# Kernel tuning notes

Hardware: AMD Instinct MI355X
Metric: run time of the kernel (lower is better)

The kernel has to match this reference:

```python
import jax, jax.numpy as jnp
import numpy as np

N = 50000      # nodes
E = 800000     # edges (avg degree 16)
G = 128        # g_dim (input feature dim)
H1 = 128       # h1_dim (RGCN output dim)
H2 = 32        # h2_dim (per-head channels)
HEADS = 4
R = 6          # num_relations
OUT = H2 * HEADS  # 128, BatchNorm width
BN_EPS = 1e-5


def setup_inputs() -> dict:
    key = jax.random.key(0)
    k = jax.random.split(key, 16)
    s = 0.05
    return {
        "node_features": jax.random.normal(k[0], (N, G), jnp.float32),
        "node_type": jax.random.randint(k[1], (N,), 0, 3),
        "edge_index": jax.random.randint(k[2], (2, E), 0, N),
        "edge_type": jax.random.randint(k[3], (E,), 0, R),
        # RGCNConv params (root_weight=True, bias=True, aggr='mean')
        "W_rel": jax.random.normal(k[4], (R, G, H1), jnp.float32) * s,
        "W_root": jax.random.normal(k[5], (G, H1), jnp.float32) * s,
        "b_rgcn": jnp.zeros((H1,), jnp.float32),
        # TransformerConv params (concat=True, root_weight=True via lin_skip)
        "Wq": jax.random.normal(k[6], (H1, OUT), jnp.float32) * s,
        "bq": jnp.zeros((OUT,), jnp.float32),
        "Wk": jax.random.normal(k[7], (H1, OUT), jnp.float32) * s,
        "bk": jnp.zeros((OUT,), jnp.float32),
        "Wv": jax.random.normal(k[8], (H1, OUT), jnp.float32) * s,
        "bv": jnp.zeros((OUT,), jnp.float32),
        "Wskip": jax.random.normal(k[9], (H1, OUT), jnp.float32) * s,
        "bskip": jnp.zeros((OUT,), jnp.float32),
        # BatchNorm1d affine params
        "bn_gamma": jnp.ones((OUT,), jnp.float32),
        "bn_beta": jnp.zeros((OUT,), jnp.float32),
    }


def _gnn_forward(node_features, edge_index, edge_type,
                 W_rel, W_root, b_rgcn,
                 Wq, bq, Wk, bk, Wv, bv, Wskip, bskip,
                 bn_gamma, bn_beta):
    src, dst = edge_index[0], edge_index[1]  # message flows src (j) -> dst (i)

    # ---- RGCNConv with mean aggregation per relation ----
    # Transform all nodes under every relation: [R, N, H1]
    xt = jnp.einsum('nd,rdo->rno', node_features, W_rel)
    msg = xt[edge_type, src]                          # [E, H1]
    seg = edge_type * N + dst                         # composite (relation, dst) segment id
    agg = jax.ops.segment_sum(msg, seg, num_segments=R * N).reshape(R, N, H1)
    cnt = jax.ops.segment_sum(jnp.ones((E,), msg.dtype), seg,
                              num_segments=R * N).reshape(R, N)
    x = node_features @ W_root + b_rgcn + (agg / jnp.maximum(cnt, 1.0)[:, :, None]).sum(0)

    # ---- TransformerConv (heads=HEADS, concat=True) ----
    q = (x @ Wq + bq).reshape(N, HEADS, H2)
    kk = (x @ Wk + bk).reshape(N, HEADS, H2)
    v = (x @ Wv + bv).reshape(N, HEADS, H2)

    score = (q[dst] * kk[src]).sum(-1) / np.sqrt(H2)  # [E, HEADS]
    m = jax.ops.segment_max(score, dst, num_segments=N)   # -inf for isolated nodes
    m = jnp.where(jnp.isfinite(m), m, 0.0)
    ex = jnp.exp(score - m[dst])
    den = jax.ops.segment_sum(ex, dst, num_segments=N)
    alpha = ex / (den[dst] + 1e-16)                   # [E, HEADS]

    out = jax.ops.segment_sum(alpha[:, :, None] * v[src], dst,
                              num_segments=N).reshape(N, OUT)
    out = out + x @ Wskip + bskip                     # skip / root connection

    # ---- BatchNorm1d (training-mode batch stats) + LeakyReLU(0.01) ----
    mu = out.mean(0)
    var = out.var(0)  # biased, as torch uses for normalization
    y = (out - mu) * jax.lax.rsqrt(var + BN_EPS) * bn_gamma + bn_beta
    return jax.nn.leaky_relu(y, negative_slope=0.01)


def reference(node_features, node_type, edge_index, edge_type,
              W_rel, W_root, b_rgcn,
              Wq, bq, Wk, bk, Wv, bv, Wskip, bskip,
              bn_gamma, bn_beta):
    # node_type is accepted but unused, matching the original forward.
    return _gnn_forward(node_features, edge_index, edge_type,
                        W_rel, W_root, b_rgcn,
                        Wq, bq, Wk, bk, Wv, bv, Wskip, bskip,
                        bn_gamma, bn_beta)
```

## Files before the change

### kernel.cpp

```cpp
#include <hip/hip_runtime.h>
#include <hip/hip_fp16.h>
#include <stdint.h>

#define G      128
#define OUTW   128
#define RNUM   6

typedef unsigned short us;
typedef _Float16 f16x8 __attribute__((ext_vector_type(8)));
typedef float    f32x4 __attribute__((ext_vector_type(4)));

__device__ inline float h2f(us u) { __half h; *(us*)&h = u; return __half2float(h); }
__device__ inline us f2h(float f) { __half h = __float2half(f); return *(us*)&h; }

union FragU { f16x8 v; ushort4 u[2]; };

__global__ void count_kernel(const int* __restrict__ ei, const int* __restrict__ et,
                             int* __restrict__ deg, int* __restrict__ cntR,
                             int N, int E) {
    int e = blockIdx.x * blockDim.x + threadIdx.x;
    if (e >= E) return;
    int dst = ei[E + e];
    int r   = et[e];
    atomicAdd(&deg[dst], 1);
    atomicAdd(&cntR[r * N + dst], 1);
}

__global__ __launch_bounds__(256)
void scan_part(const int* __restrict__ deg, int* __restrict__ bsum, int n) {
    __shared__ int s[256];
    int base = blockIdx.x * 1024, t = threadIdx.x;
    int v = 0;
    for (int j = 0; j < 4; ++j) { int idx = base + j * 256 + t; if (idx < n) v += deg[idx]; }
    s[t] = v; __syncthreads();
    for (int off = 128; off; off >>= 1) { if (t < off) s[t] += s[t + off]; __syncthreads(); }
    if (!t) bsum[blockIdx.x] = s[0];
}

__global__ void scan_top(const int* __restrict__ bsum, int* __restrict__ boff,
                         int* __restrict__ rowptr, int nb, int n) {
    int t = threadIdx.x;
    int v = (t < nb) ? bsum[t] : 0;
    for (int off = 1; off < 64; off <<= 1) {
        int y = __shfl_up(v, off);
        if (t >= off) v += y;
    }
    if (t < nb) boff[t + 1] = v;
    if (!t) boff[0] = 0;
    if (t == 63) rowptr[n] = v;
}

__global__ __launch_bounds__(256)
void scan_apply(const int* __restrict__ deg, const int* __restrict__ boff,
                int* __restrict__ rowptr, int* __restrict__ cursor, int n) {
    __shared__ int L[1024];
    __shared__ int SS[256];
    int base = blockIdx.x * 1024, t = threadIdx.x;
    for (int j = 0; j < 4; ++j) { int idx = base + j * 256 + t; L[j * 256 + t] = (idx < n) ? deg[idx] : 0; }
    __syncthreads();
    int s0 = L[t*4] + L[t*4+1] + L[t*4+2] + L[t*4+3];
    SS[t] = s0; __syncthreads();
    for (int off = 1; off < 256; off <<= 1) {
        int y = (t >= off) ? SS[t - off] : 0;
        __syncthreads();
        SS[t] += y;
        __syncthreads();
    }
    int e0 = (t ? SS[t - 1] : 0) + boff[blockIdx.x];
    int4 ov;
    int a;
    a = L[t*4+0]; ov.x = e0; e0 += a;
    a = L[t*4+1]; ov.y = e0; e0 += a;
    a = L[t*4+2]; ov.z = e0; e0 += a;
    a = L[t*4+3]; ov.w = e0; e0 += a;
    int idx0 = base + t * 4;
    if (idx0 + 3 < n) {
        *(int4*)(rowptr + idx0) = ov;
        *(int4*)(cursor + idx0) = ov;
    } else {
        int vals[4] = {ov.x, ov.y, ov.z, ov.w};
        for (int k = 0; k < 4; ++k)
            if (idx0 + k < n) { rowptr[idx0 + k] = vals[k]; cursor[idx0 + k] = vals[k]; }
    }
}

__global__ void scatter_kernel(const int* __restrict__ ei, const int* __restrict__ et,
                               int* __restrict__ cursor, unsigned int* __restrict__ epack,
                               int N, int E) {
    int e = blockIdx.x * blockDim.x + threadIdx.x;
    if (e >= E) return;
    int src = ei[e];
    int dst = ei[E + e];
    int r   = et[e];
    int pos = atomicAdd(&cursor[dst], 1);
    epack[pos] = (unsigned int)src | ((unsigned int)r << 16);
}

__global__ void xhalf_kernel(const float* __restrict__ x, us* __restrict__ xh, int total8) {
    int i = blockIdx.x * blockDim.x + threadIdx.x;
    if (i >= total8) return;
    float4 a = ((const float4*)x)[2*i];
    float4 b = ((const float4*)x)[2*i+1];
    ushort4 u0 = { f2h(a.x), f2h(a.y), f2h(a.z), f2h(a.w) };
    ushort4 u1 = { f2h(b.x), f2h(b.y), f2h(b.z), f2h(b.w) };
    ((ushort4*)xh)[2*i]   = u0;
    ((ushort4*)xh)[2*i+1] = u1;
}

__global__ __launch_bounds__(256)
void wconv_rgcn(const float* __restrict__ Wrel, const float* __restrict__ Wroot,
                ushort4* __restrict__ Btr) {
    int idx = blockIdx.x * 256 + threadIdx.x;
    if (idx >= 224 * 128) return;
    int kq = idx >> 7, n = idx & 127;
    ushort4 o;
    us* op = (us*)&o;
#pragma unroll
    for (int i = 0; i < 4; ++i) {
        int k = 4 * kq + i;
        float v = (k < 768) ? Wrel[(size_t)k * 128 + n] : Wroot[(size_t)(k - 768) * 128 + n];
        op[i] = f2h(v);
    }
    Btr[idx] = o;
}

__global__ __launch_bounds__(256)
void wconv_qkvs(const float* __restrict__ Wq, const float* __restrict__ Wk,
                const float* __restrict__ Wv, const float* __restrict__ Ws,
                ushort4* __restrict__ Btq) {
    int idx = blockIdx.x * 256 + threadIdx.x;
    if (idx >= 32 * 512) return;
    int kq = idx >> 9, n = idx & 511;
    int quad = n >> 7, nl = n & 127;
    const float* W = (quad == 0) ? Wq : (quad == 1) ? Wk : (quad == 2) ? Wv : Ws;
    ushort4 o;
    us* op = (us*)&o;
#pragma unroll
    for (int i = 0; i < 4; ++i) {
        int k = 4 * kq + i;
        op[i] = f2h(W[(size_t)k * 128 + nl]);
    }
    Btq[idx] = o;
}

__global__ __launch_bounds__(256)
void agg_kernel(const us* __restrict__ xh, const int* __restrict__ rowptr,
                const unsigned* __restrict__ epack, const int* __restrict__ cntR,
                us* __restrict__ meanh, int N) {
    const int wv = threadIdx.x >> 6, l = threadIdx.x & 63;
    const int i = blockIdx.x * 4 + wv;
    if (i >= N) return;
    const int e0 = rowptr[i], e1 = rowptr[i + 1];
    float2 a0{0,0}, a1{0,0}, a2{0,0}, a3{0,0}, a4{0,0}, a5{0,0};

#define LOADX(P) (*(const ushort2*)(xh + (size_t)((P) & 0xFFFFu) * G + 2*l))
#define ACC(P, U) { unsigned r_ = (P) >> 16; float vx_ = h2f((U).x), vy_ = h2f((U).y); \
    if      (r_ == 0) { a0.x += vx_; a0.y += vy_; } \
    else if (r_ == 1) { a1.x += vx_; a1.y += vy_; } \
    else if (r_ == 2) { a2.x += vx_; a2.y += vy_; } \
    else if (r_ == 3) { a3.x += vx_; a3.y += vy_; } \
    else if (r_ == 4) { a4.x += vx_; a4.y += vy_; } \
    else              { a5.x += vx_; a5.y += vy_; } }

    for (int base = e0; base < e1; base += 64) {
        const int nc = min(64, e1 - base);
        unsigned pv = 0;
        if (base + l < e1) pv = epack[base + l];
        int j = 0;
        for (; j + 8 <= nc; j += 8) {
            unsigned q0 = (unsigned)__shfl((int)pv, j+0);
            unsigned q1 = (unsigned)__shfl((int)pv, j+1);
            unsigned q2 = (unsigned)__shfl((int)pv, j+2);
            unsigned q3 = (unsigned)__shfl((int)pv, j+3);
            unsigned q4 = (unsigned)__shfl((int)pv, j+4);
            unsigned q5 = (unsigned)__shfl((int)pv, j+5);
            unsigned q6 = (unsigned)__shfl((int)pv, j+6);
            unsigned q7 = (unsigned)__shfl((int)pv, j+7);
            ushort2 u0 = LOADX(q0), u1 = LOADX(q1), u2 = LOADX(q2), u3 = LOADX(q3);
            ushort2 u4 = LOADX(q4), u5 = LOADX(q5), u6 = LOADX(q6), u7 = LOADX(q7);
            ACC(q0,u0); ACC(q1,u1); ACC(q2,u2); ACC(q3,u3);
            ACC(q4,u4); ACC(q5,u5); ACC(q6,u6); ACC(q7,u7);
        }
        for (; j < nc; ++j) {
            unsigned q0 = (unsigned)__shfl((int)pv, j);
            ushort2 u0 = LOADX(q0);
            ACC(q0,u0);
        }
    }
#undef ACC
#undef LOADX

    us* mrow = meanh + (size_t)i * 768 + 2*l;
#define WR(RIDX, A) { \
    float c_ = (float)cntR[(RIDX) * N + i]; \
    float s_ = 1.f / fmaxf(c_, 1.f); \
    ushort2 t_ = { f2h((A).x * s_), f2h((A).y * s_) }; \
    *(ushort2*)(mrow + (RIDX) * G) = t_; }
    WR(0, a0); WR(1, a1); WR(2, a2); WR(3, a3); WR(4, a4); WR(5, a5);
#undef WR
}

__global__ __launch_bounds__(256)
void rgcn_mfma(const us* __restrict__ meanh, const us* __restrict__ xh,
               const ushort4* __restrict__ Btr, const float* __restrict__ brg,
               us* __restrict__ xrh, int N) {
    __shared__ ushort4 Ald[16 * 64];
    const int tid = threadIdx.x;
    const int w = tid >> 6, l = tid & 63;
    const int lh = l >> 4, lm = l & 15;
    const int base = blockIdx.x * 64;
    const int arow = w * 16 + lm;

    f32x4 acc[8];
#pragma unroll
    for (int ct = 0; ct < 8; ++ct) {
        float b = brg[ct * 16 + lm];
        acc[ct] = (f32x4){b, b, b, b};
    }

    const int srow = tid >> 2;
    const int sk0  = (tid & 3) * 16;

    for (int ch = 0; ch < 14; ++ch) {
        int gi = base + srow;
        int4 d0 = {0,0,0,0}, d1 = {0,0,0,0};
        if (gi < N) {
            const us* src = (ch < 12) ? (meanh + (size_t)gi * 768 + ch * 64 + sk0)
                                      : (xh    + (size_t)gi * 128 + (ch - 12) * 64 + sk0);
            d0 = *(const int4*)src;
            d1 = *(const int4*)(src + 8);
        }
        __syncthreads();
        int kqb = sk0 >> 2;
        Ald[(kqb + 0) * 64 + srow] = ((ushort4*)&d0)[0];
        Ald[(kqb + 1) * 64 + srow] = ((ushort4*)&d0)[1];
        Ald[(kqb + 2) * 64 + srow] = ((ushort4*)&d1)[0];
        Ald[(kqb + 3) * 64 + srow] = ((ushort4*)&d1)[1];
        __syncthreads();

#pragma unroll
        for (int s = 0; s < 2; ++s) {
            FragU af;
            int kql = s * 8 + lh;
            af.u[0] = Ald[kql * 64 + arow];
            af.u[1] = Ald[(kql + 4) * 64 + arow];
            int kqg = ch * 16 + s * 8 + lh;
            const ushort4* B0 = Btr + (size_t)kqg * 128;
            const ushort4* B1 = Btr + (size_t)(kqg + 4) * 128;
#pragma unroll
            for (int ct = 0; ct < 8; ++ct) {
                FragU bf;
                bf.u[0] = B0[ct * 16 + lm];
                bf.u[1] = B1[ct * 16 + lm];
                acc[ct] = __builtin_amdgcn_mfma_f32_16x16x32_f16(af.v, bf.v, acc[ct], 0, 0, 0);
            }
        }
    }

#pragma unroll
    for (int ct = 0; ct < 8; ++ct) {
#pragma unroll
        for (int i = 0; i < 4; ++i) {
            int r = base + w * 16 + 4 * lh + i;
            if (r < N) xrh[(size_t)r * 128 + ct * 16 + lm] = f2h(acc[ct][i]);
        }
    }
}

__global__ __launch_bounds__(256)
void qkvs_mfma(const us* __restrict__ xrh, const ushort4* __restrict__ Btq,
               const float* __restrict__ bq, const float* __restrict__ bk,
               const float* __restrict__ bv, const float* __restrict__ bs,
               float* __restrict__ qs, us* __restrict__ kvh, int N) {
    __shared__ ushort4 Ald[32 * 16];
    const int tid = threadIdx.x;
    const int w = tid >> 6, l = tid & 63;
    const int lh = l >> 4, lm = l & 15;
    const int base = blockIdx.x * 16;

    {
        int row = tid >> 4, k0 = (tid & 15) * 8;
        int gi = base + row;
        int4 d0 = {0,0,0,0};
        if (gi < N) d0 = *(const int4*)(xrh + (size_t)gi * 128 + k0);
        int kqb = k0 >> 2;
        Ald[(kqb + 0) * 16 + row] = ((ushort4*)&d0)[0];
        Ald[(kqb + 1) * 16 + row] = ((ushort4*)&d0)[1];
    }
    __syncthreads();

    const float* bias = (w == 0) ? bq : (w == 1) ? bk : (w == 2) ? bv : bs;
    f32x4 acc[8];
#pragma unroll
    for (int ct = 0; ct < 8; ++ct) {
        float b = bias[ct * 16 + lm];
        acc[ct] = (f32x4){b, b, b, b};
    }

#pragma unroll
    for (int s = 0; s < 4; ++s) {
        FragU af;
        int kq = s * 8 + lh;
        af.u[0] = Ald[kq * 16 + lm];
        af.u[1] = Ald[(kq + 4) * 16 + lm];
        const ushort4* B0 = Btq + (size_t)kq * 512 + w * 128;
        const ushort4* B1 = Btq + (size_t)(kq + 4) * 512 + w * 128;
#pragma unroll
        for (int ct = 0; ct < 8; ++ct) {
            FragU bf;
            bf.u[0] = B0[ct * 16 + lm];
            bf.u[1] = B1[ct * 16 + lm];
            acc[ct] = __builtin_amdgcn_mfma_f32_16x16x32_f16(af.v, bf.v, acc[ct], 0, 0, 0);
        }
    }

    if (w == 0 || w == 3) {
        int off = (w == 0) ? 0 : 128;
#pragma unroll
        for (int ct = 0; ct < 8; ++ct)
#pragma unroll
            for (int i = 0; i < 4; ++i) {
                int r = base + 4 * lh + i;
                if (r < N) qs[(size_t)r * 256 + off + ct * 16 + lm] = acc[ct][i];
            }
    } else {
        int off = (w == 1) ? 0 : 2;
#pragma unroll
        for (int ct = 0; ct < 8; ++ct)
#pragma unroll
            for (int i = 0; i < 4; ++i) {
                int r = base + 4 * lh + i;
                int col = ct * 16 + lm;
                if (r < N) kvh[(size_t)r * 256 + (col >> 1) * 4 + (col & 1) + off] = f2h(acc[ct][i]);
            }
    }
}

__global__ __launch_bounds__(256)
void attn_kernel(const float* __restrict__ qs, const us* __restrict__ kvh,
                 const int* __restrict__ rowptr, const unsigned* __restrict__ epack,
                 float* __restrict__ out, int N) {
    const int wv = threadIdx.x >> 6, l = threadIdx.x & 63;
    const int i = blockIdx.x * 4 + wv;
    if (i >= N) return;
    const float QS = 0.17677669529663687f;

    float2 q2 = *(const float2*)(qs + (size_t)i * 256 + 2*l);
    q2.x *= QS; q2.y *= QS;

    float m = -INFINITY, den = 0.f;
    float2 acc = {0.f, 0.f};
    const int e0 = rowptr[i], e1 = rowptr[i + 1];

#define KVLOAD(P) (*(const ushort4*)(kvh + (size_t)((P) & 0xFFFFu) * 256 + 4*l))
#define SCORE(U, S) { \
    float s_ = q2.x * h2f((U).x) + q2.y * h2f((U).y); \
    s_ += __shfl_xor(s_, 1, 16); s_ += __shfl_xor(s_, 2, 16); \
    s_ += __shfl_xor(s_, 4, 16); s_ += __shfl_xor(s_, 8, 16); \
    S = s_; }

    for (int base = e0; base < e1; base += 64) {
        const int nc = min(64, e1 - base);
        unsigned pv = 0;
        if (base + l < e1) pv = epack[base + l];
        int j = 0;
        for (; j + 4 <= nc; j += 4) {
            unsigned p0 = (unsigned)__shfl((int)pv, j+0);
            unsigned p1 = (unsigned)__shfl((int)pv, j+1);
            unsigned p2 = (unsigned)__shfl((int)pv, j+2);
            unsigned p3 = (unsigned)__shfl((int)pv, j+3);
            ushort4 k0 = KVLOAD(p0), k1 = KVLOAD(p1), k2 = KVLOAD(p2), k3 = KVLOAD(p3);
            float s0, s1, s2, s3;
            SCORE(k0, s0); SCORE(k1, s1); SCORE(k2, s2); SCORE(k3, s3);
            float mx = fmaxf(fmaxf(fmaxf(s0, s1), fmaxf(s2, s3)), m);
            float rs = __expf(m - mx);
            float p0e = __expf(s0 - mx), p1e = __expf(s1 - mx);
            float p2e = __expf(s2 - mx), p3e = __expf(s3 - mx);
            den = den * rs + ((p0e + p1e) + (p2e + p3e));
            acc.x = acc.x * rs + p0e*h2f(k0.z) + p1e*h2f(k1.z) + p2e*h2f(k2.z) + p3e*h2f(k3.z);
            acc.y = acc.y * rs + p0e*h2f(k0.w) + p1e*h2f(k1.w) + p2e*h2f(k2.w) + p3e*h2f(k3.w);
            m = mx;
        }
        for (; j < nc; ++j) {
            unsigned p0 = (unsigned)__shfl((int)pv, j);
            ushort4 k0 = KVLOAD(p0);
            float s0; SCORE(k0, s0);
            float mx = fmaxf(m, s0);
            float rs = __expf(m - mx);
            float pe = __expf(s0 - mx);
            den = den * rs + pe;
            acc.x = acc.x * rs + pe * h2f(k0.z);
            acc.y = acc.y * rs + pe * h2f(k0.w);
            m = mx;
        }
    }
#undef SCORE
#undef KVLOAD

    float inv = 1.f / (den + 1e-16f);
    float2 sk = *(const float2*)(qs + (size_t)i * 256 + 128 + 2*l);
    float2 o = { acc.x * inv + sk.x, acc.y * inv + sk.y };
    *(float2*)(out + (size_t)i * OUTW + 2*l) = o;
}

__global__ __launch_bounds__(256)
void bnreduce_kernel(const float* __restrict__ out, float* __restrict__ bnS,
                     float* __restrict__ bnQ, int N) {
    __shared__ float S[256], Q[256];
    const int tid = threadIdx.x;
    const int col = tid & 127, half = tid >> 7;
    float s = 0.f, q = 0.f;
    for (int r = blockIdx.x * 2 + half; r < N; r += gridDim.x * 2) {
        float v = out[(size_t)r * OUTW + col];
        s += v; q += v * v;
    }
    S[tid] = s; Q[tid] = q;
    __syncthreads();
    if (tid < 128) {
        atomicAdd(&bnS[tid], S[tid] + S[tid + 128]);
        atomicAdd(&bnQ[tid], Q[tid] + Q[tid + 128]);
    }
}

__global__ void bnstats_kernel(const float* __restrict__ bnS, const float* __restrict__ bnQ,
                               const float* __restrict__ gamma, const float* __restrict__ beta,
                               float* __restrict__ bnA, float* __restrict__ bnB, int N) {
    int c = threadIdx.x;
    if (c >= 128) return;
    float fN  = (float)N;
    float mu  = bnS[c] / fN;
    float var = bnQ[c] / fN - mu * mu;
    float rv  = rsqrtf(var + 1e-5f);
    float A   = rv * gamma[c];
    bnA[c] = A;
    bnB[c] = beta[c] - mu * A;
}

__global__ void apply_kernel(float* __restrict__ out, const float* __restrict__ bnA,
                             const float* __restrict__ bnB, int total4) {
    int idx4 = blockIdx.x * blockDim.x + threadIdx.x;
    if (idx4 >= total4) return;
    float4 v = ((const float4*)out)[idx4];
    int c0 = (idx4 * 4) & 127;
    float y;
    y = bnA[c0    ] * v.x + bnB[c0    ]; v.x = (y > 0.f) ? y : 0.01f * y;
    y = bnA[c0 + 1] * v.y + bnB[c0 + 1]; v.y = (y > 0.f) ? y : 0.01f * y;
    y = bnA[c0 + 2] * v.z + bnB[c0 + 2]; v.z = (y > 0.f) ? y : 0.01f * y;
    y = bnA[c0 + 3] * v.w + bnB[c0 + 3]; v.w = (y > 0.f) ? y : 0.01f * y;
    ((float4*)out)[idx4] = v;
}

static inline char* alignp(char* p) {
    return (char*)(((uintptr_t)p + 255) & ~(uintptr_t)255);
}

extern "C" void kernel_launch(void* const* d_in, const int* in_sizes, int n_in,
                              void* d_out, int out_size, void* d_ws, size_t ws_size,
                              hipStream_t stream) {
    const float* x     = (const float*)d_in[0];
    const int*   ei    = (const int*)  d_in[2];
    const int*   et    = (const int*)  d_in[3];
    const float* Wrel  = (const float*)d_in[4];
    const float* Wroot = (const float*)d_in[5];
    const float* brg   = (const float*)d_in[6];
    const float* Wq    = (const float*)d_in[7];
    const float* bq    = (const float*)d_in[8];
    const float* Wk    = (const float*)d_in[9];
    const float* bk    = (const float*)d_in[10];
    const float* Wv    = (const float*)d_in[11];
    const float* bv    = (const float*)d_in[12];
    const float* Wsk   = (const float*)d_in[13];
    const float* bsk   = (const float*)d_in[14];
    const float* gamma = (const float*)d_in[15];
    const float* beta  = (const float*)d_in[16];
    float* out = (float*)d_out;

    const int N = in_sizes[0] / G;
    const int E = in_sizes[3];
    const int NB_SCAN = (N + 1023) / 1024;

    char* w = (char*)d_ws;
    int* deg   = (int*)w;            w += (size_t)N * 4;
    int* cntR  = (int*)w;            w += (size_t)RNUM * N * 4;
    float* bnS = (float*)w;          w += 128 * 4;
    float* bnQ = (float*)w;          w += 128 * 4;
    float* bnA = (float*)w;          w += 128 * 4;
    float* bnB = (float*)w;          w += 128 * 4;
    size_t zero_bytes = (size_t)(w - (char*)d_ws);
    w = alignp(w);
    int* bsum  = (int*)w;            w += 64 * 4;
    int* boff  = (int*)w;            w += 65 * 4;
    w = alignp(w);
    int* rowptr = (int*)w;           w += (size_t)(N + 1) * 4;
    w = alignp(w);
    int* cursor = (int*)w;           w += (size_t)N * 4;
    w = alignp(w);
    unsigned* epack = (unsigned*)w;  w += (size_t)E * 4;
    w = alignp(w);
    us* xh     = (us*)w;             w += (size_t)N * G * 2;
    w = alignp(w);
    us* xrh    = (us*)w;             w += (size_t)N * OUTW * 2;
    w = alignp(w);
    ushort4* Btr = (ushort4*)w;      w += (size_t)224 * 128 * 8;
    w = alignp(w);
    ushort4* Btq = (ushort4*)w;      w += (size_t)32 * 512 * 8;
    w = alignp(w);
    us*    meanh = (us*)w;
    float* qs    = (float*)w;
    us*    kvh   = (us*)(w + (size_t)N * 256 * 4);

    hipMemsetAsync(d_ws, 0, zero_bytes, stream);

    int eb = (E + 255) / 256;
    count_kernel<<<eb, 256, 0, stream>>>(ei, et, deg, cntR, N, E);

    scan_part<<<NB_SCAN, 256, 0, stream>>>(deg, bsum, N);
    scan_top<<<1, 64, 0, stream>>>(bsum, boff, rowptr, NB_SCAN, N);
    scan_apply<<<NB_SCAN, 256, 0, stream>>>(deg, boff, rowptr, cursor, N);

    scatter_kernel<<<eb, 256, 0, stream>>>(ei, et, cursor, epack, N, E);

    int total8 = N * G / 8;
    xhalf_kernel<<<(total8 + 255) / 256, 256, 0, stream>>>(x, xh, total8);

    wconv_rgcn<<<112, 256, 0, stream>>>(Wrel, Wroot, Btr);
    wconv_qkvs<<<64, 256, 0, stream>>>(Wq, Wk, Wv, Wsk, Btq);

    agg_kernel<<<(N + 3) / 4, 256, 0, stream>>>(xh, rowptr, epack, cntR, meanh, N);

    rgcn_mfma<<<(N + 63) / 64, 256, 0, stream>>>(meanh, xh, Btr, brg, xrh, N);

    qkvs_mfma<<<(N + 15) / 16, 256, 0, stream>>>(xrh, Btq, bq, bk, bv, bsk, qs, kvh, N);

    attn_kernel<<<(N + 3) / 4, 256, 0, stream>>>(qs, kvh, rowptr, epack, out, N);

    bnreduce_kernel<<<200, 256, 0, stream>>>(out, bnS, bnQ, N);
    bnstats_kernel<<<1, 128, 0, stream>>>(bnS, bnQ, gamma, beta, bnA, bnB, N);

    int total4 = N * OUTW / 4;
    apply_kernel<<<(total4 + 255) / 256, 256, 0, stream>>>(out, bnA, bnB, total4);
}
```

Measured before the change: 509.8 us.

## Sort edges by (dst, relation) and fuse RGCN aggregation into MFMA kernel

Edges are now bucketed into CSR segments keyed by (dst, relation), which replaces the per-edge relation branch and the separate per-relation count array. The mean aggregation is moved into the RGCN MFMA kernel, so each block gathers neighbour features straight into LDS tiles per relation chunk. This removes the intermediate meanh buffer of 768 halves per node and one kernel launch. In exchange the CSR is six times larger, the scan grows to a 512-thread top level, and each wave walks edges serially with scalar readfirstlane loads, which lowers gather parallelism inside the MFMA kernel.

```diff
diff --git a/kernel.cpp b/kernel.cpp
--- a/kernel.cpp
+++ b/kernel.cpp
@@ -16,47 +16,51 @@
 union FragU { f16x8 v; ushort4 u[2]; };
 
 __global__ void count_kernel(const int* __restrict__ ei, const int* __restrict__ et,
-                             int* __restrict__ deg, int* __restrict__ cntR,
-                             int N, int E) {
+                             int* __restrict__ segcnt, int N, int E) {
     int e = blockIdx.x * blockDim.x + threadIdx.x;
     if (e >= E) return;
     int dst = ei[E + e];
     int r   = et[e];
-    atomicAdd(&deg[dst], 1);
-    atomicAdd(&cntR[r * N + dst], 1);
-}
-
-__global__ __launch_bounds__(256)
-void scan_part(const int* __restrict__ deg, int* __restrict__ bsum, int n) {
+    atomicAdd(&segcnt[dst * RNUM + r], 1);
+}
+
+__global__ __launch_bounds__(256)
+void scan_part(const int* __restrict__ cnt, int* __restrict__ bsum, int n) {
     __shared__ int s[256];
     int base = blockIdx.x * 1024, t = threadIdx.x;
     int v = 0;
-    for (int j = 0; j < 4; ++j) { int idx = base + j * 256 + t; if (idx < n) v += deg[idx]; }
+    for (int j = 0; j < 4; ++j) { int idx = base + j * 256 + t; if (idx < n) v += cnt[idx]; }
     s[t] = v; __syncthreads();
     for (int off = 128; off; off >>= 1) { if (t < off) s[t] += s[t + off]; __syncthreads(); }
     if (!t) bsum[blockIdx.x] = s[0];
 }
 
-__global__ void scan_top(const int* __restrict__ bsum, int* __restrict__ boff,
-                         int* __restrict__ rowptr, int nb, int n) {
+__global__ __launch_bounds__(512)
+void scan_top(const int* __restrict__ bsum, int* __restrict__ boff,
+              int* __restrict__ segptr, int nb, int n) {
+    __shared__ int s[512];
     int t = threadIdx.x;
     int v = (t < nb) ? bsum[t] : 0;
-    for (int off = 1; off < 64; off <<= 1) {
-        int y = __shfl_up(v, off);
-        if (t >= off) v += y;
-    }
-    if (t < nb) boff[t + 1] = v;
+    s[t] = v;
+    __syncthreads();
+    for (int off = 1; off < 512; off <<= 1) {
+        int y = (t >= off) ? s[t - off] : 0;
+        __syncthreads();
+        s[t] += y;
+        __syncthreads();
+    }
+    if (t < nb) boff[t + 1] = s[t];
     if (!t) boff[0] = 0;
-    if (t == 63) rowptr[n] = v;
-}
-
-__global__ __launch_bounds__(256)
-void scan_apply(const int* __restrict__ deg, const int* __restrict__ boff,
-                int* __restrict__ rowptr, int* __restrict__ cursor, int n) {
+    if (t == nb - 1) segptr[n] = s[t];
+}
+
+__global__ __launch_bounds__(256)
+void scan_apply(const int* __restrict__ cnt, const int* __restrict__ boff,
+                int* __restrict__ segptr, int* __restrict__ cursor, int n) {
     __shared__ int L[1024];
     __shared__ int SS[256];
     int base = blockIdx.x * 1024, t = threadIdx.x;
-    for (int j = 0; j < 4; ++j) { int idx = base + j * 256 + t; L[j * 256 + t] = (idx < n) ? deg[idx] : 0; }
+    for (int j = 0; j < 4; ++j) { int idx = base + j * 256 + t; L[j * 256 + t] = (idx < n) ? cnt[idx] : 0; }
     __syncthreads();
     int s0 = L[t*4] + L[t*4+1] + L[t*4+2] + L[t*4+3];
     SS[t] = s0; __syncthreads();
@@ -75,25 +79,25 @@
     a = L[t*4+3]; ov.w = e0; e0 += a;
     int idx0 = base + t * 4;
     if (idx0 + 3 < n) {
-        *(int4*)(rowptr + idx0) = ov;
+        *(int4*)(segptr + idx0) = ov;
         *(int4*)(cursor + idx0) = ov;
     } else {
         int vals[4] = {ov.x, ov.y, ov.z, ov.w};
         for (int k = 0; k < 4; ++k)
-            if (idx0 + k < n) { rowptr[idx0 + k] = vals[k]; cursor[idx0 + k] = vals[k]; }
+            if (idx0 + k < n) { segptr[idx0 + k] = vals[k]; cursor[idx0 + k] = vals[k]; }
     }
 }
 
 __global__ void scatter_kernel(const int* __restrict__ ei, const int* __restrict__ et,
-                               int* __restrict__ cursor, unsigned int* __restrict__ epack,
+                               int* __restrict__ cursor, unsigned* __restrict__ esrc,
                                int N, int E) {
     int e = blockIdx.x * blockDim.x + threadIdx.x;
     if (e >= E) return;
     int src = ei[e];
     int dst = ei[E + e];
     int r   = et[e];
-    int pos = atomicAdd(&cursor[dst], 1);
-    epack[pos] = (unsigned int)src | ((unsigned int)r << 16);
+    int pos = atomicAdd(&cursor[dst * RNUM + r], 1);
+    esrc[pos] = (unsigned)src;
 }
 
 __global__ void xhalf_kernel(const float* __restrict__ x, us* __restrict__ xh, int total8) {
@@ -144,67 +148,10 @@
 }
 
 __global__ __launch_bounds__(256)
-void agg_kernel(const us* __restrict__ xh, const int* __restrict__ rowptr,
-                const unsigned* __restrict__ epack, const int* __restrict__ cntR,
-                us* __restrict__ meanh, int N) {
-    const int wv = threadIdx.x >> 6, l = threadIdx.x & 63;
-    const int i = blockIdx.x * 4 + wv;
-    if (i >= N) return;
-    const int e0 = rowptr[i], e1 = rowptr[i + 1];
-    float2 a0{0,0}, a1{0,0}, a2{0,0}, a3{0,0}, a4{0,0}, a5{0,0};
-
-#define LOADX(P) (*(const ushort2*)(xh + (size_t)((P) & 0xFFFFu) * G + 2*l))
-#define ACC(P, U) { unsigned r_ = (P) >> 16; float vx_ = h2f((U).x), vy_ = h2f((U).y); \
-    if      (r_ == 0) { a0.x += vx_; a0.y += vy_; } \
-    else if (r_ == 1) { a1.x += vx_; a1.y += vy_; } \
-    else if (r_ == 2) { a2.x += vx_; a2.y += vy_; } \
-    else if (r_ == 3) { a3.x += vx_; a3.y += vy_; } \
-    else if (r_ == 4) { a4.x += vx_; a4.y += vy_; } \
-    else              { a5.x += vx_; a5.y += vy_; } }
-
-    for (int base = e0; base < e1; base += 64) {
-        const int nc = min(64, e1 - base);
-        unsigned pv = 0;
-        if (base + l < e1) pv = epack[base + l];
-        int j = 0;
-        for (; j + 8 <= nc; j += 8) {
-            unsigned q0 = (unsigned)__shfl((int)pv, j+0);
-            unsigned q1 = (unsigned)__shfl((int)pv, j+1);
-            unsigned q2 = (unsigned)__shfl((int)pv, j+2);
-            unsigned q3 = (unsigned)__shfl((int)pv, j+3);
-            unsigned q4 = (unsigned)__shfl((int)pv, j+4);
-            unsigned q5 = (unsigned)__shfl((int)pv, j+5);
-            unsigned q6 = (unsigned)__shfl((int)pv, j+6);
-            unsigned q7 = (unsigned)__shfl((int)pv, j+7);
-            ushort2 u0 = LOADX(q0), u1 = LOADX(q1), u2 = LOADX(q2), u3 = LOADX(q3);
-            ushort2 u4 = LOADX(q4), u5 = LOADX(q5), u6 = LOADX(q6), u7 = LOADX(q7);
-            ACC(q0,u0); ACC(q1,u1); ACC(q2,u2); ACC(q3,u3);
-            ACC(q4,u4); ACC(q5,u5); ACC(q6,u6); ACC(q7,u7);
-        }
-        for (; j < nc; ++j) {
-            unsigned q0 = (unsigned)__shfl((int)pv, j);
-            ushort2 u0 = LOADX(q0);
-            ACC(q0,u0);
-        }
-    }
-#undef ACC
-#undef LOADX
-
-    us* mrow = meanh + (size_t)i * 768 + 2*l;
-#define WR(RIDX, A) { \
-    float c_ = (float)cntR[(RIDX) * N + i]; \
-    float s_ = 1.f / fmaxf(c_, 1.f); \
-    ushort2 t_ = { f2h((A).x * s_), f2h((A).y * s_) }; \
-    *(ushort2*)(mrow + (RIDX) * G) = t_; }
-    WR(0, a0); WR(1, a1); WR(2, a2); WR(3, a3); WR(4, a4); WR(5, a5);
-#undef WR
-}
-
-__global__ __launch_bounds__(256)
-void rgcn_mfma(const us* __restrict__ meanh, const us* __restrict__ xh,
-               const ushort4* __restrict__ Btr, const float* __restrict__ brg,
-               us* __restrict__ xrh, int N) {
-    __shared__ ushort4 Ald[16 * 64];
+void rgcn_fused(const us* __restrict__ xh, const int* __restrict__ segptr,
+                const unsigned* __restrict__ esrc, const ushort4* __restrict__ Btr,
+                const float* __restrict__ brg, us* __restrict__ xrh, int N) {
+    __shared__ ushort4 Ald[64][33];
     const int tid = threadIdx.x;
     const int w = tid >> 6, l = tid & 63;
     const int lh = l >> 4, lm = l & 15;
@@ -218,33 +165,53 @@
         acc[ct] = (f32x4){b, b, b, b};
     }
 
-    const int srow = tid >> 2;
-    const int sk0  = (tid & 3) * 16;
-
-    for (int ch = 0; ch < 14; ++ch) {
-        int gi = base + srow;
-        int4 d0 = {0,0,0,0}, d1 = {0,0,0,0};
-        if (gi < N) {
-            const us* src = (ch < 12) ? (meanh + (size_t)gi * 768 + ch * 64 + sk0)
-                                      : (xh    + (size_t)gi * 128 + (ch - 12) * 64 + sk0);
-            d0 = *(const int4*)src;
-            d1 = *(const int4*)(src + 8);
+    for (int ch = 0; ch < 7; ++ch) {
+        __syncthreads();
+        for (int j = 0; j < 16; ++j) {
+            const int row = w * 16 + j;
+            const int i = base + row;
+            float2 a = {0.f, 0.f};
+            if (i < N) {
+                if (ch < 6) {
+                    int s0 = __builtin_amdgcn_readfirstlane(segptr[i * RNUM + ch]);
+                    int s1 = __builtin_amdgcn_readfirstlane(segptr[i * RNUM + ch + 1]);
+                    int e = s0;
+                    for (; e + 4 <= s1; e += 4) {
+                        unsigned q0 = __builtin_amdgcn_readfirstlane(esrc[e]);
+                        unsigned q1 = __builtin_amdgcn_readfirstlane(esrc[e + 1]);
+                        unsigned q2 = __builtin_amdgcn_readfirstlane(esrc[e + 2]);
+                        unsigned q3 = __builtin_amdgcn_readfirstlane(esrc[e + 3]);
+                        ushort2 u0 = *(const ushort2*)(xh + (size_t)q0 * G + 2 * l);
+                        ushort2 u1 = *(const ushort2*)(xh + (size_t)q1 * G + 2 * l);
+                        ushort2 u2 = *(const ushort2*)(xh + (size_t)q2 * G + 2 * l);
+                        ushort2 u3 = *(const ushort2*)(xh + (size_t)q3 * G + 2 * l);
+                        a.x += (h2f(u0.x) + h2f(u1.x)) + (h2f(u2.x) + h2f(u3.x));
+                        a.y += (h2f(u0.y) + h2f(u1.y)) + (h2f(u2.y) + h2f(u3.y));
+                    }
+                    for (; e < s1; ++e) {
+                        unsigned q0 = __builtin_amdgcn_readfirstlane(esrc[e]);
+                        ushort2 u0 = *(const ushort2*)(xh + (size_t)q0 * G + 2 * l);
+                        a.x += h2f(u0.x);
+                        a.y += h2f(u0.y);
+                    }
+                    float sc = 1.f / fmaxf((float)(s1 - s0), 1.f);
+                    a.x *= sc; a.y *= sc;
+                } else {
+                    ushort2 u = *(const ushort2*)(xh + (size_t)i * G + 2 * l);
+                    a.x = h2f(u.x); a.y = h2f(u.y);
+                }
+            }
+            ushort2 t = { f2h(a.x), f2h(a.y) };
+            *((ushort2*)&Ald[row][l >> 1] + (l & 1)) = t;
         }
         __syncthreads();
-        int kqb = sk0 >> 2;
-        Ald[(kqb + 0) * 64 + srow] = ((ushort4*)&d0)[0];
-        Ald[(kqb + 1) * 64 + srow] = ((ushort4*)&d0)[1];
-        Ald[(kqb + 2) * 64 + srow] = ((ushort4*)&d1)[0];
-        Ald[(kqb + 3) * 64 + srow] = ((ushort4*)&d1)[1];
-        __syncthreads();
-
-#pragma unroll
-        for (int s = 0; s < 2; ++s) {
+#pragma unroll
+        for (int s = 0; s < 4; ++s) {
             FragU af;
-            int kql = s * 8 + lh;
-            af.u[0] = Ald[kql * 64 + arow];
-            af.u[1] = Ald[(kql + 4) * 64 + arow];
-            int kqg = ch * 16 + s * 8 + lh;
+            const int kql = s * 8 + lh;
+            af.u[0] = Ald[arow][kql];
+            af.u[1] = Ald[arow][kql + 4];
+            const int kqg = ch * 32 + kql;
             const ushort4* B0 = Btr + (size_t)kqg * 128;
             const ushort4* B1 = Btr + (size_t)(kqg + 4) * 128;
 #pragma unroll
@@ -338,7 +305,7 @@
 
 __global__ __launch_bounds__(256)
 void attn_kernel(const float* __restrict__ qs, const us* __restrict__ kvh,
-                 const int* __restrict__ rowptr, const unsigned* __restrict__ epack,
+                 const int* __restrict__ segptr, const unsigned* __restrict__ esrc,
                  float* __restrict__ out, int N) {
     const int wv = threadIdx.x >> 6, l = threadIdx.x & 63;
     const int i = blockIdx.x * 4 + wv;
@@ -350,9 +317,9 @@
 
     float m = -INFINITY, den = 0.f;
     float2 acc = {0.f, 0.f};
-    const int e0 = rowptr[i], e1 = rowptr[i + 1];
-
-#define KVLOAD(P) (*(const ushort4*)(kvh + (size_t)((P) & 0xFFFFu) * 256 + 4*l))
+    const int e0 = segptr[(size_t)i * RNUM], e1 = segptr[(size_t)i * RNUM + RNUM];
+
+#define KVLOAD(P) (*(const ushort4*)(kvh + (size_t)(P) * 256 + 4*l))
 #define SCORE(U, S) { \
     float s_ = q2.x * h2f((U).x) + q2.y * h2f((U).y); \
     s_ += __shfl_xor(s_, 1, 16); s_ += __shfl_xor(s_, 2, 16); \
@@ -362,7 +329,7 @@
     for (int base = e0; base < e1; base += 64) {
         const int nc = min(64, e1 - base);
         unsigned pv = 0;
-        if (base + l < e1) pv = epack[base + l];
+        if (base + l < e1) pv = esrc[base + l];
         int j = 0;
         for (; j + 4 <= nc; j += 4) {
             unsigned p0 = (unsigned)__shfl((int)pv, j+0);
@@ -477,25 +444,25 @@
 
     const int N = in_sizes[0] / G;
     const int E = in_sizes[3];
-    const int NB_SCAN = (N + 1023) / 1024;
+    const int NSEG = N * RNUM;
+    const int NB_SCAN = (NSEG + 1023) / 1024;
 
     char* w = (char*)d_ws;
-    int* deg   = (int*)w;            w += (size_t)N * 4;
-    int* cntR  = (int*)w;            w += (size_t)RNUM * N * 4;
+    int* segcnt = (int*)w;           w += (size_t)NSEG * 4;
     float* bnS = (float*)w;          w += 128 * 4;
     float* bnQ = (float*)w;          w += 128 * 4;
     float* bnA = (float*)w;          w += 128 * 4;
     float* bnB = (float*)w;          w += 128 * 4;
     size_t zero_bytes = (size_t)(w - (char*)d_ws);
     w = alignp(w);
-    int* bsum  = (int*)w;            w += 64 * 4;
-    int* boff  = (int*)w;            w += 65 * 4;
-    w = alignp(w);
-    int* rowptr = (int*)w;           w += (size_t)(N + 1) * 4;
-    w = alignp(w);
-    int* cursor = (int*)w;           w += (size_t)N * 4;
-    w = alignp(w);
-    unsigned* epack = (unsigned*)w;  w += (size_t)E * 4;
+    int* bsum  = (int*)w;            w += 512 * 4;
+    int* boff  = (int*)w;            w += 513 * 4;
+    w = alignp(w);
+    int* segptr = (int*)w;           w += (size_t)(NSEG + 1) * 4;
+    w = alignp(w);
+    int* cursor = (int*)w;           w += (size_t)NSEG * 4;
+    w = alignp(w);
+    unsigned* esrc = (unsigned*)w;   w += (size_t)E * 4;
     w = alignp(w);
     us* xh     = (us*)w;             w += (size_t)N * G * 2;
     w = alignp(w);
@@ -505,20 +472,20 @@
     w = alignp(w);
     ushort4* Btq = (ushort4*)w;      w += (size_t)32 * 512 * 8;
     w = alignp(w);
-    us*    meanh = (us*)w;
-    float* qs    = (float*)w;
-    us*    kvh   = (us*)(w + (size_t)N * 256 * 4);
+    float* qs  = (float*)w;          w += (size_t)N * 256 * 4;
+    w = alignp(w);
+    us* kvh    = (us*)w;             w += (size_t)N * 256 * 2;
 
     hipMemsetAsync(d_ws, 0, zero_bytes, stream);
 
     int eb = (E + 255) / 256;
-    count_kernel<<<eb, 256, 0, stream>>>(ei, et, deg, cntR, N, E);
-
-    scan_part<<<NB_SCAN, 256, 0, stream>>>(deg, bsum, N);
-    scan_top<<<1, 64, 0, stream>>>(bsum, boff, rowptr, NB_SCAN, N);
-    scan_apply<<<NB_SCAN, 256, 0, stream>>>(deg, boff, rowptr, cursor, N);
-
-    scatter_kernel<<<eb, 256, 0, stream>>>(ei, et, cursor, epack, N, E);
+    count_kernel<<<eb, 256, 0, stream>>>(ei, et, segcnt, N, E);
+
+    scan_part<<<NB_SCAN, 256, 0, stream>>>(segcnt, bsum, NSEG);
+    scan_top<<<1, 512, 0, stream>>>(bsum, boff, segptr, NB_SCAN, NSEG);
+    scan_apply<<<NB_SCAN, 256, 0, stream>>>(segcnt, boff, segptr, cursor, NSEG);
+
+    scatter_kernel<<<eb, 256, 0, stream>>>(ei, et, cursor, esrc, N, E);
 
     int total8 = N * G / 8;
     xhalf_kernel<<<(total8 + 255) / 256, 256, 0, stream>>>(x, xh, total8);
@@ -526,13 +493,11 @@
     wconv_rgcn<<<112, 256, 0, stream>>>(Wrel, Wroot, Btr);
     wconv_qkvs<<<64, 256, 0, stream>>>(Wq, Wk, Wv, Wsk, Btq);
 
-    agg_kernel<<<(N + 3) / 4, 256, 0, stream>>>(xh, rowptr, epack, cntR, meanh, N);
-
-    rgcn_mfma<<<(N + 63) / 64, 256, 0, stream>>>(meanh, xh, Btr, brg, xrh, N);
+    rgcn_fused<<<(N + 63) / 64, 256, 0, stream>>>(xh, segptr, esrc, Btr, brg, xrh, N);
 
     qkvs_mfma<<<(N + 15) / 16, 256, 0, stream>>>(xrh, Btq, bq, bk, bv, bsk, qs, kvh, N);
 
-    attn_kernel<<<(N + 3) / 4, 256, 0, stream>>>(qs, kvh, rowptr, epack, out, N);
+    attn_kernel<<<(N + 3) / 4, 256, 0, stream>>>(qs, kvh, segptr, esrc, out, N);
 
     bnreduce_kernel<<<200, 256, 0, stream>>>(out, bnS, bnQ, N);
     bnstats_kernel<<<1, 128, 0, stream>>>(bnS, bnQ, gamma, beta, bnA, bnB, N);
```

After: 525.9 us. +3.2%, slower.
